# Kernel tuning notes

Measured on AMD Instinct MI355X. Metric: run time of the kernel, lower is better.

## Reference

```python
import jax, jax.numpy as jnp
import numpy as np

FILTER_LEN = 32
SCALE = float(np.sqrt(10 ** (-15 / 10)))  # expected_SI_power_dB = -15


def _fir_valid(x, w):
    """Valid cross-correlation along W axis. x: [B,H,W,1], w: [L] -> [B,H,W-L+1,1].
    Matches Keras Conv2D(kernel_size=(1,L), padding='valid') (cross-correlation)."""
    B, H, W, _ = x.shape
    L = w.shape[0]
    xr = x.reshape(B * H, W, 1)
    k = w.reshape(L, 1, 1)  # (spatial, in, out)
    y = jax.lax.conv_general_dilated(xr, k, window_strides=(1,), padding='VALID',
                                     dimension_numbers=('NWC', 'WIO', 'NWC'))
    return y.reshape(B, H, W - L + 1, 1)


def setup_inputs() -> dict:
    key = jax.random.key(0)
    ks = jax.random.split(key, 10)
    B, H, W = 16, 1, 262144
    f32 = jnp.float32
    return {
        'x_real': jax.random.normal(ks[0], (B, H, W, 1), f32),
        'x_imag': jax.random.normal(ks[1], (B, H, W, 1), f32),
        'w1_pre': jax.random.normal(ks[2], (1, 8), f32) * 0.5,
        'w2_pre': jax.random.normal(ks[3], (8, 1), f32) * 0.5,
        'w_fir_r': jax.random.normal(ks[4], (FILTER_LEN,), f32) * 0.1,
        'w_fir_i': jax.random.normal(ks[5], (FILTER_LEN,), f32) * 0.1,
        'w1_post': jax.random.normal(ks[6], (1, 8), f32) * 0.5,
        'b1_post': jax.random.normal(ks[7], (8,), f32) * 0.1,
        'w2_post': jax.random.normal(ks[8], (8, 1), f32) * 0.5,
        'b2_post': jax.random.normal(ks[9], (1,), f32) * 0.1,
    }


def reference(x_real, x_imag, w1_pre, w2_pre, w_fir_r, w_fir_i,
              w1_post, b1_post, w2_post, b2_post):
    # --- pre nonlinearity on magnitude (1x1 conv MLP: 1 -> 8 tanh -> 1) ---
    x_mag = jnp.sqrt(x_real * x_real + x_imag * x_imag)      # [B,H,W,1]
    x_phase = jnp.arctan2(x_imag, x_real)                    # [B,H,W,1]
    h = jnp.tanh(jnp.einsum('bhwc,cf->bhwf', x_mag, w1_pre))  # [B,H,W,8]
    m = jnp.einsum('bhwf,fc->bhwc', h, w2_pre)               # [B,H,W,1]
    xh_r = m * jnp.cos(x_phase)
    xh_i = m * jnp.sin(x_phase)
    # --- complex FIR (length-32, valid) via 4 real convs ---
    zr = _fir_valid(xh_r, w_fir_r) - _fir_valid(xh_i, w_fir_i)
    zi = _fir_valid(xh_i, w_fir_r) + _fir_valid(xh_r, w_fir_i)
    # --- post nonlinearity on magnitude (1x1 conv MLP: 1 -> 8 relu -> 1) ---
    z_mag = jnp.sqrt(zr * zr + zi * zi)
    z_phase = jnp.arctan2(zi, zr)
    g = jax.nn.relu(jnp.einsum('bhwc,cf->bhwf', z_mag, w1_post) + b1_post)
    zm = jnp.einsum('bhwf,fc->bhwc', g, w2_post) + b2_post
    yr = SCALE * zm * jnp.cos(z_phase)
    yi = SCALE * zm * jnp.sin(z_phase)
    # complex output represented as [real, imag] on last axis: [B,H,W-31,2]
    return jnp.concatenate([yr, yi], axis=-1)
```

## Files before the change

### kernel.cpp

```cpp
#include <hip/hip_runtime.h>

#define TILE   2048
#define NLOAD  (TILE + 32)
#define NBLK   (NLOAD / 4)
#define WIDTH  262144
#define OUTW   (WIDTH - 31)
#define SCALE_V 0.17782794100389229f
#define LOG2E_X2 2.8853900817779268f

__device__ __forceinline__ int swz(int b) { return b ^ ((b >> 3) & 7); }

__global__ __launch_bounds__(256) void fused_hammer(
    const float* __restrict__ xr_g,   const float* __restrict__ xi_g,
    const float* __restrict__ w1_pre, const float* __restrict__ w2_pre,
    const float* __restrict__ wfr,    const float* __restrict__ wfi,
    const float* __restrict__ w1_post,const float* __restrict__ b1_post,
    const float* __restrict__ w2_post,const float* __restrict__ b2_post,
    float* __restrict__ out)
{
    __shared__ __align__(16) float s_r[NLOAD];
    __shared__ __align__(16) float s_i[NLOAD];

    const int tid    = threadIdx.x;
    const int tstart = blockIdx.x * TILE;
    const int brow   = blockIdx.y;
    const long rowbase = (long)brow * WIDTH;

    float w1v[8], w2v[8];
    float sumw2 = 0.f;
#pragma unroll
    for (int f = 0; f < 8; ++f) {
        w1v[f] = LOG2E_X2 * w1_pre[f];
        w2v[f] = w2_pre[f];
        sumw2 += w2_pre[f];
    }

    for (int p = tid; p < NBLK; p += 256) {
        const int g = tstart + 4 * p;
        float4 vr, vi;
        if (g + 3 < WIDTH) {
            vr = *(const float4*)(xr_g + rowbase + g);
            vi = *(const float4*)(xi_g + rowbase + g);
        } else {
            float rr[4], ii[4];
#pragma unroll
            for (int e = 0; e < 4; ++e) {
                const int gg = g + e;
                rr[e] = (gg < WIDTH) ? xr_g[rowbase + gg] : 0.f;
                ii[e] = (gg < WIDTH) ? xi_g[rowbase + gg] : 0.f;
            }
            vr = make_float4(rr[0], rr[1], rr[2], rr[3]);
            vi = make_float4(ii[0], ii[1], ii[2], ii[3]);
        }
        float hr[4], hi[4];
        const float* vrf = &vr.x;
        const float* vif = &vi.x;
#pragma unroll
        for (int e = 0; e < 4; ++e) {
            const float r  = vrf[e], im = vif[e];
            const float sq = fmaf(r, r, im * im);
            const float rs = (sq > 0.f) ? __builtin_amdgcn_rsqf(sq) : 0.f;
            const float mag = sq * rs;
            float tw = 0.f;
#pragma unroll
            for (int f = 0; f < 8; ++f) {
                const float e2 = __builtin_amdgcn_exp2f(mag * w1v[f]);
                const float tt = __builtin_amdgcn_rcpf(e2 + 1.0f);
                tw = fmaf(w2v[f], tt, tw);
            }
            const float m = sumw2 - 2.0f * tw;
            const float s = m * rs;
            hr[e] = s * r;
            hi[e] = s * im;
        }
        const int ph = 4 * swz(p);
        *(float4*)&s_r[ph] = make_float4(hr[0], hr[1], hr[2], hr[3]);
        *(float4*)&s_i[ph] = make_float4(hi[0], hi[1], hi[2], hi[3]);
    }
    __syncthreads();

    const int base = tid * 8;
    float accr[8], acci[8];
#pragma unroll
    for (int j = 0; j < 8; ++j) { accr[j] = 0.f; acci[j] = 0.f; }

#pragma unroll
    for (int tc = 0; tc < 4; ++tc) {
        float wrf[16], wif[16];
#pragma unroll
        for (int q = 0; q < 4; ++q) {
            const int B  = 2 * tid + 2 * tc + q;
            const int ph = 4 * swz(B);
            *(float4*)&wrf[4 * q] = *(const float4*)&s_r[ph];
            *(float4*)&wif[4 * q] = *(const float4*)&s_i[ph];
        }
#pragma unroll
        for (int tt = 0; tt < 8; ++tt) {
            const float fr = wfr[8 * tc + tt];
            const float fi = wfi[8 * tc + tt];
#pragma unroll
            for (int j = 0; j < 8; ++j) {
                const float ar = wrf[j + tt];
                const float ai = wif[j + tt];
                accr[j] = fmaf(fr,  ar, accr[j]);
                accr[j] = fmaf(-fi, ai, accr[j]);
                acci[j] = fmaf(fr,  ai, acci[j]);
                acci[j] = fmaf(fi,  ar, acci[j]);
            }
        }
    }

    float w1p[8], b1p[8], w2p[8];
#pragma unroll
    for (int f = 0; f < 8; ++f) { w1p[f] = w1_post[f]; b1p[f] = b1_post[f]; w2p[f] = w2_post[f]; }
    const float b2p = b2_post[0];

#pragma unroll
    for (int j = 0; j < 8; ++j) {
        const int o = tstart + base + j;
        if (o < OUTW) {
            const float zr  = accr[j], zi = acci[j];
            const float zsq = fmaf(zr, zr, zi * zi);
            const float rs  = (zsq > 0.f) ? __builtin_amdgcn_rsqf(zsq) : 0.f;
            const float zmag = zsq * rs;
            float zm = b2p;
#pragma unroll
            for (int f = 0; f < 8; ++f) {
                const float gfv = fmaf(zmag, w1p[f], b1p[f]);
                zm = fmaf(fmaxf(gfv, 0.f), w2p[f], zm);
            }
            const float t = SCALE_V * zm * rs;
            float2 o2;
            o2.x = (zsq > 0.f) ? t * zr : SCALE_V * zm;
            o2.y = t * zi;
            *(float2*)&out[((long)brow * OUTW + o) * 2] = o2;
        }
    }
}

extern "C" void kernel_launch(void* const* d_in, const int* in_sizes, int n_in,
                              void* d_out, int out_size, void* d_ws, size_t ws_size,
                              hipStream_t stream) {
    const int blocks_w = (OUTW + TILE - 1) / TILE;
    dim3 grid(blocks_w, 16);
    fused_hammer<<<grid, 256, 0, stream>>>(
        (const float*)d_in[0], (const float*)d_in[1],
        (const float*)d_in[2], (const float*)d_in[3],
        (const float*)d_in[4], (const float*)d_in[5],
        (const float*)d_in[6], (const float*)d_in[7],
        (const float*)d_in[8], (const float*)d_in[9],
        (float*)d_out);
}
```

Baseline: 123.5 us.

## Compute complex FIR with split-fp16 MFMA Toeplitz matrix multiplies

```diff
diff --git a/kernel.cpp b/kernel.cpp
--- a/kernel.cpp
+++ b/kernel.cpp
@@ -1,16 +1,24 @@
 #include <hip/hip_runtime.h>
 
 #define TILE   2048
-#define NLOAD  (TILE + 32)
-#define NBLK   (NLOAD / 4)
+#define NS     2096
 #define WIDTH  262144
 #define OUTW   (WIDTH - 31)
 #define SCALE_V 0.17782794100389229f
 #define LOG2E_X2 2.8853900817779268f
 
-__device__ __forceinline__ int swz(int b) { return b ^ ((b >> 3) & 7); }
+typedef _Float16 half8  __attribute__((ext_vector_type(8)));
+typedef _Float16 half4v __attribute__((ext_vector_type(4)));
+typedef float    floatx4 __attribute__((ext_vector_type(4)));
 
-__global__ __launch_bounds__(256) void fused_hammer(
+__device__ __forceinline__ float wload(const float* __restrict__ w, int t) {
+    return (t >= 0 && t < 32) ? w[t] : 0.0f;
+}
+
+#define MFMA16(A, B, C) __builtin_amdgcn_mfma_f32_16x16x32_f16((A), (B), (C), 0, 0, 0)
+
+
+__global__ __launch_bounds__(256) void fused_hammer_mfma(
     const float* __restrict__ xr_g,   const float* __restrict__ xi_g,
     const float* __restrict__ w1_pre, const float* __restrict__ w2_pre,
     const float* __restrict__ wfr,    const float* __restrict__ wfi,
@@ -18,24 +26,53 @@
     const float* __restrict__ w2_post,const float* __restrict__ b2_post,
     float* __restrict__ out)
 {
-    __shared__ __align__(16) float s_r[NLOAD];
-    __shared__ __align__(16) float s_i[NLOAD];
+    __shared__ __align__(16) _Float16 s_rh[NS];
+    __shared__ __align__(16) _Float16 s_rl[NS];
+    __shared__ __align__(16) _Float16 s_ih[NS];
+    __shared__ __align__(16) _Float16 s_il[NS];
 
     const int tid    = threadIdx.x;
+    const int lane   = tid & 63;
+    const int wv     = tid >> 6;
     const int tstart = blockIdx.x * TILE;
     const int brow   = blockIdx.y;
     const long rowbase = (long)brow * WIDTH;
 
-    float w1v[8], w2v[8];
-    float sumw2 = 0.f;
+    float w1v[8], w2v[8], sumw2 = 0.f;
 #pragma unroll
     for (int f = 0; f < 8; ++f) {
         w1v[f] = LOG2E_X2 * w1_pre[f];
         w2v[f] = w2_pre[f];
         sumw2 += w2_pre[f];
     }
+    float w1p[8], b1p[8], w2p[8];
+#pragma unroll
+    for (int f = 0; f < 8; ++f) { w1p[f] = w1_post[f]; b1p[f] = b1_post[f]; w2p[f] = w2_post[f]; }
+    const float b2p = b2_post[0];
 
-    for (int p = tid; p < NBLK; p += 256) {
+    const int jA = lane & 15;
+    const int kg = lane >> 4;
+    half8 A1r_h, A1r_l, A1mi_h, A1mi_l, A1i_h, A1i_l, A2r_h, A2r_l, A2i_h, A2i_l;
+#pragma unroll
+    for (int jj = 0; jj < 8; ++jj) {
+        const int k  = 8 * kg + jj;
+        const int t1 = k - jA;
+        const float wr1 = wload(wfr, t1);
+        const float wi1 = wload(wfi, t1);
+        const int t2 = (k < 16) ? (k + 32 - jA) : (k + 16 - jA);
+        const float wr2 = wload(wfr, t2);
+        const float wi2 = wload(wfi, t2);
+        const float a2r = (k < 16) ? wr2 : -wi2;
+        const float a2i = (k < 16) ? wi2 : wr2;
+        _Float16 h;
+        h = (_Float16)wr1;   A1r_h[jj]  = h; A1r_l[jj]  = (_Float16)(wr1 - (float)h);
+        h = (_Float16)(-wi1);A1mi_h[jj] = h; A1mi_l[jj] = (_Float16)(-wi1 - (float)h);
+        h = (_Float16)wi1;   A1i_h[jj]  = h; A1i_l[jj]  = (_Float16)(wi1 - (float)h);
+        h = (_Float16)a2r;   A2r_h[jj]  = h; A2r_l[jj]  = (_Float16)(a2r - (float)h);
+        h = (_Float16)a2i;   A2i_h[jj]  = h; A2i_l[jj]  = (_Float16)(a2i - (float)h);
+    }
+
+    for (int p = tid; p < NS / 4; p += 256) {
         const int g = tstart + 4 * p;
         float4 vr, vi;
         if (g + 3 < WIDTH) {
@@ -52,9 +89,9 @@
             vr = make_float4(rr[0], rr[1], rr[2], rr[3]);
             vi = make_float4(ii[0], ii[1], ii[2], ii[3]);
         }
-        float hr[4], hi[4];
         const float* vrf = &vr.x;
         const float* vif = &vi.x;
+        half4v rh, rl, ih, il;
 #pragma unroll
         for (int e = 0; e < 4; ++e) {
             const float r  = vrf[e], im = vif[e];
@@ -65,75 +102,71 @@
 #pragma unroll
             for (int f = 0; f < 8; ++f) {
                 const float e2 = __builtin_amdgcn_exp2f(mag * w1v[f]);
-                const float tt = __builtin_amdgcn_rcpf(e2 + 1.0f);
-                tw = fmaf(w2v[f], tt, tw);
+                tw = fmaf(w2v[f], __builtin_amdgcn_rcpf(e2 + 1.0f), tw);
             }
             const float m = sumw2 - 2.0f * tw;
             const float s = m * rs;
-            hr[e] = s * r;
-            hi[e] = s * im;
+            const float xhr = s * r;
+            const float xhi = s * im;
+            const _Float16 hr = (_Float16)xhr;
+            const _Float16 hi = (_Float16)xhi;
+            rh[e] = hr; rl[e] = (_Float16)(xhr - (float)hr);
+            ih[e] = hi; il[e] = (_Float16)(xhi - (float)hi);
         }
-        const int ph = 4 * swz(p);
-        *(float4*)&s_r[ph] = make_float4(hr[0], hr[1], hr[2], hr[3]);
-        *(float4*)&s_i[ph] = make_float4(hi[0], hi[1], hi[2], hi[3]);
+        *(half4v*)&s_rh[4 * p] = rh;
+        *(half4v*)&s_rl[4 * p] = rl;
+        *(half4v*)&s_ih[4 * p] = ih;
+        *(half4v*)&s_il[4 * p] = il;
     }
     __syncthreads();
 
-    const int base = tid * 8;
-    float accr[8], acci[8];
 #pragma unroll
-    for (int j = 0; j < 8; ++j) { accr[j] = 0.f; acci[j] = 0.f; }
+    for (int tt = 0; tt < 2; ++tt) {
+        const int base_o = 512 * wv + 256 * tt;
+        const int i1 = base_o + 16 * jA + 8 * kg;
+        const half8 Bxr_h = *(const half8*)&s_rh[i1];
+        const half8 Bxi_h = *(const half8*)&s_ih[i1];
+        const half8 Bxr_l = *(const half8*)&s_rl[i1];
+        const half8 Bxi_l = *(const half8*)&s_il[i1];
+        const int i2 = base_o + 16 * jA + 32 + 8 * (kg & 1);
+        const _Float16* srcH = (kg < 2) ? s_rh : s_ih;
+        const _Float16* srcL = (kg < 2) ? s_rl : s_il;
+        const half8 Bmx_h = *(const half8*)&srcH[i2];
+        const half8 Bmx_l = *(const half8*)&srcL[i2];
 
+        floatx4 accr = {0.f, 0.f, 0.f, 0.f};
+        floatx4 acci = {0.f, 0.f, 0.f, 0.f};
+        accr = MFMA16(A1r_h,  Bxr_h, accr);  acci = MFMA16(A1i_h,  Bxr_h, acci);
+        accr = MFMA16(A1mi_h, Bxi_h, accr);  acci = MFMA16(A1r_h,  Bxi_h, acci);
+        accr = MFMA16(A2r_h,  Bmx_h, accr);  acci = MFMA16(A2i_h,  Bmx_h, acci);
+        accr = MFMA16(A1r_h,  Bxr_l, accr);  acci = MFMA16(A1i_h,  Bxr_l, acci);
+        accr = MFMA16(A1mi_h, Bxi_l, accr);  acci = MFMA16(A1r_h,  Bxi_l, acci);
+        accr = MFMA16(A2r_h,  Bmx_l, accr);  acci = MFMA16(A2i_h,  Bmx_l, acci);
+        accr = MFMA16(A1r_l,  Bxr_h, accr);  acci = MFMA16(A1i_l,  Bxr_h, acci);
+        accr = MFMA16(A1mi_l, Bxi_h, accr);  acci = MFMA16(A1r_l,  Bxi_h, acci);
+        accr = MFMA16(A2r_l,  Bmx_h, accr);  acci = MFMA16(A2i_l,  Bmx_h, acci);
+
+        const int obase = tstart + base_o + 16 * jA + 4 * kg;
 #pragma unroll
-    for (int tc = 0; tc < 4; ++tc) {
-        float wrf[16], wif[16];
+        for (int r = 0; r < 4; ++r) {
+            const int o = obase + r;
+            if (o < OUTW) {
+                const float zr  = accr[r], zi = acci[r];
+                const float zsq = fmaf(zr, zr, zi * zi);
+                const float rs  = (zsq > 0.f) ? __builtin_amdgcn_rsqf(zsq) : 0.f;
+                const float zmag = zsq * rs;
+                float zm = b2p;
 #pragma unroll
-        for (int q = 0; q < 4; ++q) {
-            const int B  = 2 * tid + 2 * tc + q;
-            const int ph = 4 * swz(B);
-            *(float4*)&wrf[4 * q] = *(const float4*)&s_r[ph];
-            *(float4*)&wif[4 * q] = *(const float4*)&s_i[ph];
-        }
-#pragma unroll
-        for (int tt = 0; tt < 8; ++tt) {
-            const float fr = wfr[8 * tc + tt];
-            const float fi = wfi[8 * tc + tt];
-#pragma unroll
-            for (int j = 0; j < 8; ++j) {
-                const float ar = wrf[j + tt];
-                const float ai = wif[j + tt];
-                accr[j] = fmaf(fr,  ar, accr[j]);
-                accr[j] = fmaf(-fi, ai, accr[j]);
-                acci[j] = fmaf(fr,  ai, acci[j]);
-                acci[j] = fmaf(fi,  ar, acci[j]);
+                for (int f = 0; f < 8; ++f) {
+                    const float gfv = fmaf(zmag, w1p[f], b1p[f]);
+                    zm = fmaf(fmaxf(gfv, 0.f), w2p[f], zm);
+                }
+                const float t = SCALE_V * zm * rs;
+                float2 o2;
+                o2.x = (zsq > 0.f) ? t * zr : SCALE_V * zm;
+                o2.y = t * zi;
+                *(float2*)&out[((long)brow * OUTW + o) * 2] = o2;
             }
-        }
-    }
-
-    float w1p[8], b1p[8], w2p[8];
-#pragma unroll
-    for (int f = 0; f < 8; ++f) { w1p[f] = w1_post[f]; b1p[f] = b1_post[f]; w2p[f] = w2_post[f]; }
-    const float b2p = b2_post[0];
-
-#pragma unroll
-    for (int j = 0; j < 8; ++j) {
-        const int o = tstart + base + j;
-        if (o < OUTW) {
-            const float zr  = accr[j], zi = acci[j];
-            const float zsq = fmaf(zr, zr, zi * zi);
-            const float rs  = (zsq > 0.f) ? __builtin_amdgcn_rsqf(zsq) : 0.f;
-            const float zmag = zsq * rs;
-            float zm = b2p;
-#pragma unroll
-            for (int f = 0; f < 8; ++f) {
-                const float gfv = fmaf(zmag, w1p[f], b1p[f]);
-                zm = fmaf(fmaxf(gfv, 0.f), w2p[f], zm);
-            }
-            const float t = SCALE_V * zm * rs;
-            float2 o2;
-            o2.x = (zsq > 0.f) ? t * zr : SCALE_V * zm;
-            o2.y = t * zi;
-            *(float2*)&out[((long)brow * OUTW + o) * 2] = o2;
         }
     }
 }
@@ -143,7 +176,7 @@
                               hipStream_t stream) {
     const int blocks_w = (OUTW + TILE - 1) / TILE;
     dim3 grid(blocks_w, 16);
-    fused_hammer<<<grid, 256, 0, stream>>>(
+    fused_hammer_mfma<<<grid, 256, 0, stream>>>(
         (const float*)d_in[0], (const float*)d_in[1],
         (const float*)d_in[2], (const float*)d_in[3],
         (const float*)d_in[4], (const float*)d_in[5],
```

New measurement: 113.9 us. 1.08x faster.
